# Optimization experiments

Hardware: AMD Instinct MI355X
Metric: run time of the kernel (lower is better)

Reference implementation:

```python
import jax, jax.numpy as jnp
import numpy as np
import math

IN_F, OUT_F = 4096, 4096
ORDER, TENSOR_RANK = 4, 8
LEAF_A = math.ceil(IN_F ** (1.0 / ORDER))   # 8
LEAF_B = math.ceil(OUT_F ** (1.0 / ORDER))  # 8


def setup_inputs() -> dict:
    key = jax.random.key(0)
    k1, k2, k3, k4 = jax.random.split(key, 4)
    x = jax.random.normal(k1, (8, 2048, IN_F), dtype=jnp.float32)
    weight = jax.random.normal(k2, (OUT_F, IN_F), dtype=jnp.float32) * 0.02
    bias = jax.random.normal(k3, (OUT_F,), dtype=jnp.float32) * 0.02
    # reset_parameters: gain for leaky_relu(sqrt(5)) = sqrt(2/(1+5)); std = gain / in_features**(1/order)
    gain = math.sqrt(2.0 / (1.0 + 5.0))
    std = gain / (IN_F ** (1.0 / ORDER))
    weight_leafs = jax.random.uniform(
        k4, (ORDER, TENSOR_RANK, LEAF_A, LEAF_B), dtype=jnp.float32,
        minval=-std, maxval=std)
    return {"x": x, "weight": weight, "bias": bias, "weight_leafs": weight_leafs}


def _reproduce_weight(weight_leafs):
    # Original einsum 'lij,rmn->rimjn' sums the FIRST operand over its leading
    # (rank) axis; chained through both stages + final .sum(0), every leaf is
    # summed over tensor_rank. Exact math = nested Kronecker of the rank-summed
    # leaves, sliced to [:in_features, :out_features].
    s = weight_leafs.sum(axis=1)  # (4, a, b)
    a, b = LEAF_A, LEAF_B
    z1 = jnp.einsum('ij,mn->imjn', s[0], s[1]).reshape(a * a, b * b)
    z2 = jnp.einsum('ij,mn->imjn', s[2], s[3]).reshape(a * a, b * b)
    zzz = jnp.einsum('ij,mn->imjn', z1, z2).reshape(a ** 4, b ** 4)
    return zzz[:IN_F, :OUT_F]  # (in_features, out_features)


def reference(x, weight, bias, weight_leafs):
    tensor_weight = _reproduce_weight(weight_leafs)       # (in, out)
    full_weight = weight + tensor_weight.T                # (out, in)
    # F.linear: x @ W^T + b
    return jnp.einsum('bsi,oi->bso', x, full_weight) + bias
```

## Files before the change

kernel.cpp:

```cpp
#include <hip/hip_runtime.h>
#include <hip/hip_bf16.h>
#include <stdint.h>

typedef __attribute__((ext_vector_type(8))) __bf16 bf16x8;
typedef __attribute__((ext_vector_type(4))) float f32x4;

#define IN_F   4096
#define OUT_F  4096
#define M_ROWS 16384

static __device__ __forceinline__ unsigned short f2bf(float f) {
    unsigned int u = __float_as_uint(f);
    u += 0x7FFFu + ((u >> 16) & 1u);
    return (unsigned short)(u >> 16);
}

#define PREP_WBLK 1366
#define PREP_NBLK 4096

__global__ __launch_bounds__(256) void prep_kernel(
    const float* __restrict__ weight, const float* __restrict__ leafs,
    const float* __restrict__ x,
    unsigned short* __restrict__ wb, unsigned short* __restrict__ xbuf)
{
    const int t = threadIdx.x;
    if (blockIdx.x < PREP_WBLK) {
        __shared__ float s[4][8][8];
        {
            const int o = t >> 6, a = (t >> 3) & 7, b = t & 7;
            float acc = 0.f;
            #pragma unroll
            for (int r = 0; r < 8; ++r)
                acc += leafs[o * 512 + r * 64 + a * 8 + b];
            s[o][a][b] = acc;
        }
        __syncthreads();

        const int total = (OUT_F * IN_F) / 8;
        for (int idx = blockIdx.x * 256 + t; idx < total; idx += PREP_WBLK * 256) {
            const int n  = idx >> 9;
            const int kg = idx & 511;
            const int n0 = n >> 9, n1 = (n >> 6) & 7, n2 = (n >> 3) & 7, n3 = n & 7;
            const int k0 = kg >> 6, k1 = (kg >> 3) & 7, k2 = kg & 7;
            const float p = s[0][k0][n0] * s[1][k1][n1] * s[2][k2][n2];
            const float4* wp = (const float4*)(weight + (size_t)n * IN_F + kg * 8);
            const float4 w0 = wp[0], w1 = wp[1];
            const float wv[8] = {w0.x, w0.y, w0.z, w0.w, w1.x, w1.y, w1.z, w1.w};
            unsigned int pk[4];
            #pragma unroll
            for (int j = 0; j < 4; ++j) {
                unsigned int lo = f2bf(wv[2*j]   + p * s[3][2*j]  [n3]);
                unsigned int hi = f2bf(wv[2*j+1] + p * s[3][2*j+1][n3]);
                pk[j] = lo | (hi << 16);
            }
            *reinterpret_cast<uint4*>(wb + (size_t)n * IN_F + kg * 8) =
                make_uint4(pk[0], pk[1], pk[2], pk[3]);
        }
    } else {
        const long long n8 = (long long)M_ROWS * IN_F / 8;
        const int xblocks = PREP_NBLK - PREP_WBLK;
        for (long long idx = (long long)(blockIdx.x - PREP_WBLK) * 256 + t;
             idx < n8; idx += (long long)xblocks * 256) {
            const float4* xp = (const float4*)(x + idx * 8);
            const float4 a = xp[0], b = xp[1];
            const float v[8] = {a.x, a.y, a.z, a.w, b.x, b.y, b.z, b.w};
            unsigned int pk[4];
            #pragma unroll
            for (int j = 0; j < 4; ++j)
                pk[j] = (unsigned int)f2bf(v[2*j]) | ((unsigned int)f2bf(v[2*j+1]) << 16);
            *reinterpret_cast<uint4*>(xbuf + idx * 8) =
                make_uint4(pk[0], pk[1], pk[2], pk[3]);
        }
    }
}

#define BK 64
#define NT 64

#define PANEL_A(b,kk) (ldsb + ((b)*2+(kk))*16384)
#define PANEL_B(b,kk) (ldsb + 65536 + ((b)*2+(kk))*16384)

#define GLL(src, dst) __builtin_amdgcn_global_load_lds( \
    (const __attribute__((address_space(1))) void*)(src), \
    (__attribute__((address_space(3))) void*)(dst), 16, 0, 0)

#define STAGE_A(b, kk, ko) do { \
    GLL(sA1 + (ko) + (kk)*32,          PANEL_A(b,kk) + d1); \
    GLL(sA1 + 524288 + (ko) + (kk)*32, PANEL_A(b,kk) + d1 + 8192); } while(0)
#define STAGE_B(b, kk, ko) do { \
    GLL(sB1 + (ko) + (kk)*32,          PANEL_B(b,kk) + d1); \
    GLL(sB1 + 524288 + (ko) + (kk)*32, PANEL_B(b,kk) + d1 + 8192); } while(0)

#define SB0  __builtin_amdgcn_sched_barrier(0)
#define BAR  __builtin_amdgcn_s_barrier()
#define PRI1 __builtin_amdgcn_s_setprio(1)
#define PRI0 __builtin_amdgcn_s_setprio(0)
#define WLG4 asm volatile("s_waitcnt lgkmcnt(4)" ::: "memory")
#define WLG8 asm volatile("s_waitcnt lgkmcnt(8)" ::: "memory")
#define WLG0 asm volatile("s_waitcnt lgkmcnt(0)" ::: "memory")
#define WVM2 asm volatile("s_waitcnt vmcnt(2)" ::: "memory")
#define WVM0 asm volatile("s_waitcnt vmcnt(0)" ::: "memory")

#define LDA(dst, BUF, KK, MH) do { _Pragma("unroll") \
    for (int i_ = 0; i_ < 4; ++i_) \
        dst[i_] = *(const bf16x8*)(aB + ((BUF)*32768 + (KK)*16384 + ((MH)*4+i_)*1024)); } while(0)
#define LDB(dst, BUF, KK) do { _Pragma("unroll") \
    for (int i_ = 0; i_ < 4; ++i_) \
        dst[i_] = *(const bf16x8*)(bB + ((BUF)*32768 + (KK)*16384 + i_*1024)); } while(0)
#define MMB(AS, BS, MH) do { _Pragma("unroll") \
    for (int m_ = 0; m_ < 4; ++m_) { _Pragma("unroll") \
    for (int n_ = 0; n_ < 4; ++n_) \
        acc[(MH)*4+m_][n_] = __builtin_amdgcn_mfma_f32_16x16x32_bf16( \
            AS[m_], BS[n_], acc[(MH)*4+m_][n_], 0, 0, 0); } } while(0)

#define TILE(BUF, KO, PF) do { \
     \
    LDA(aQ, BUF, 0, 1); \
    if (PF) STAGE_A((BUF)^1, 0, KO); \
    SB0; WLG4; SB0; \
    PRI1; MMB(aP, bP, 0); PRI0; SB0; \
    if (PF) { WVM2; } else { WVM0; } \
    BAR; SB0; \
     \
    LDA(aP, BUF, 1, 0); \
    LDB(bQ, BUF, 1); \
    if (PF) STAGE_B((BUF)^1, 0, KO); \
    SB0; WLG8; SB0; \
    PRI1; MMB(aQ, bP, 1); PRI0; SB0; \
    BAR; SB0; \
     \
    LDA(aQ, BUF, 1, 1); \
    if (PF) STAGE_A((BUF)^1, 1, KO); \
    SB0; WLG4; SB0; \
    PRI1; MMB(aP, bQ, 0); PRI0; SB0; \
    if (PF) { WVM2; } else { WVM0; } \
    BAR; SB0; \
     \
    if (PF) { LDA(aP, (BUF)^1, 0, 0); LDB(bP, (BUF)^1, 0); STAGE_B((BUF)^1, 1, KO); SB0; WLG8; } \
    else    { SB0; WLG0; } \
    SB0; \
    PRI1; MMB(aQ, bQ, 1); PRI0; SB0; \
    BAR; SB0; \
} while (0)

__global__ __launch_bounds__(512, 2) void gemm8_kernel(
    const unsigned short* __restrict__ xb,
    const unsigned short* __restrict__ wb,
    const float* __restrict__ bias,
    float* __restrict__ out)
{
    __shared__ unsigned short lds_us[65536];
    char* const ldsb = (char*)lds_us;

    const int t    = threadIdx.x;
    const int wave = t >> 6;
    const int lane = t & 63;
    const int lr   = lane & 15;
    const int kq   = lane >> 4;
    const int wr   = wave >> 2;
    const int wcn  = wave & 3;
    const int sx   = (lr & 6) << 3;

    const int bid  = blockIdx.x;
    const int swzb = (bid & 7) * 128 + (bid >> 3);
    const int bm   = (swzb >> 4) * 256;
    const int bn   = (swzb & 15) * 256;

    const int c1 = t;
    const int r1 = c1 >> 2;
    const int q1 = ((c1 & 3) * 16) ^ ((r1 & 6) << 3);
    const unsigned short* sA1 = xb + (size_t)(bm + r1) * IN_F + (q1 >> 1);
    const unsigned short* sB1 = wb + (size_t)(bn + r1) * IN_F + (q1 >> 1);
    const int d1 = c1 * 16;

    const char* aB = ldsb + (wr * 128 + lr) * 64 + ((kq * 16) ^ sx);
    const char* bB = ldsb + 65536 + (wcn * 64 + lr) * 64 + ((kq * 16) ^ sx);

    f32x4 acc[8][4] = {};
    bf16x8 aP[4], aQ[4], bP[4], bQ[4];

    STAGE_A(0, 0, 0); STAGE_B(0, 0, 0); STAGE_A(0, 1, 0); STAGE_B(0, 1, 0);
    asm volatile("s_waitcnt vmcnt(4)" ::: "memory");
    BAR; SB0;
    LDA(aP, 0, 0, 0);
    LDB(bP, 0, 0);

    #pragma unroll 1
    for (int tt = 0; tt < NT - 2; tt += 2) {
        const int ko0 = (tt + 1) * BK;
        const int ko1 = (tt + 2) * BK;
        TILE(0, ko0, true);
        TILE(1, ko1, true);
    }
    TILE(0, (NT - 1) * BK, true);
    TILE(1, 0, false);

    #pragma unroll
    for (int n = 0; n < 4; ++n) {
        const int col = bn + wcn * 64 + n * 16 + lr;
        const float bv = bias[col];
        #pragma unroll
        for (int m = 0; m < 8; ++m) {
            const size_t rb = (size_t)(bm + wr * 128 + m * 16 + kq * 4) * OUT_F + col;
            #pragma unroll
            for (int j = 0; j < 4; ++j)
                out[rb + (size_t)j * OUT_F] = acc[m][n][j] + bv;
        }
    }
}

#define FBM 128
#define FBN 128
#define FBK 32

__global__ __launch_bounds__(256) void gemm_fb_kernel(
    const float* __restrict__ xf,
    const unsigned short* __restrict__ wb,
    const float* __restrict__ bias,
    float* __restrict__ out)
{
    __shared__ unsigned short As[FBM * FBK];
    __shared__ unsigned short Bs[FBN * FBK];

    const int t    = threadIdx.x;
    const int wave = t >> 6;
    const int lane = t & 63;
    const int lr   = lane & 15;
    const int kq   = lane >> 4;
    const int wr   = wave >> 1;
    const int wc   = wave & 1;

    const int bm = blockIdx.x * FBM;
    const int bn = blockIdx.y * FBN;
    const int srow = t >> 2;
    const int scol = (t & 3) * 8;

    f32x4 acc[4][4] = {};

    for (int kt = 0; kt < IN_F; kt += FBK) {
        #pragma unroll
        for (int g = 0; g < 2; ++g) {
            const int row = srow + g * 64;
            const float4* xp = (const float4*)(xf + (size_t)(bm + row) * IN_F + kt + scol);
            const float4 a0 = xp[0], a1 = xp[1];
            const float v[8] = {a0.x, a0.y, a0.z, a0.w, a1.x, a1.y, a1.z, a1.w};
            unsigned int pk[4];
            #pragma unroll
            for (int j = 0; j < 4; ++j)
                pk[j] = (unsigned int)f2bf(v[2*j]) | ((unsigned int)f2bf(v[2*j+1]) << 16);
            *reinterpret_cast<uint4*>(&As[row * FBK + scol]) =
                make_uint4(pk[0], pk[1], pk[2], pk[3]);
        }
        {
            const unsigned short* gb0 = wb + (size_t)(bn + srow) * IN_F + kt + scol;
            const unsigned short* gb1 = gb0 + (size_t)64 * IN_F;
            GLL(gb0, Bs + srow * FBK + scol);
            GLL(gb1, Bs + (64 + srow) * FBK + scol);
        }
        __syncthreads();

        bf16x8 af[4], bfr[4];
        #pragma unroll
        for (int m = 0; m < 4; ++m)
            af[m] = *reinterpret_cast<const bf16x8*>(As + (wr * 64 + m * 16 + lr) * FBK + kq * 8);
        #pragma unroll
        for (int n = 0; n < 4; ++n)
            bfr[n] = *reinterpret_cast<const bf16x8*>(Bs + (wc * 64 + n * 16 + lr) * FBK + kq * 8);

        #pragma unroll
        for (int m = 0; m < 4; ++m)
            #pragma unroll
            for (int n = 0; n < 4; ++n)
                acc[m][n] = __builtin_amdgcn_mfma_f32_16x16x32_bf16(af[m], bfr[n], acc[m][n], 0, 0, 0);

        __syncthreads();
    }

    const int crow0 = kq * 4;
    #pragma unroll
    for (int n = 0; n < 4; ++n) {
        const int col = bn + wc * 64 + n * 16 + lr;
        const float bv = bias[col];
        #pragma unroll
        for (int m = 0; m < 4; ++m) {
            const int rowb = bm + wr * 64 + m * 16 + crow0;
            #pragma unroll
            for (int j = 0; j < 4; ++j)
                out[(size_t)(rowb + j) * OUT_F + col] = acc[m][n][j] + bv;
        }
    }
}

extern "C" void kernel_launch(void* const* d_in, const int* in_sizes, int n_in,
                              void* d_out, int out_size, void* d_ws, size_t ws_size,
                              hipStream_t stream) {
    const float* x      = (const float*)d_in[0];
    const float* weight = (const float*)d_in[1];
    const float* bias   = (const float*)d_in[2];
    const float* leafs  = (const float*)d_in[3];
    float* out = (float*)d_out;

    unsigned short* wb = (unsigned short*)d_ws;
    unsigned short* xbuf = (unsigned short*)((char*)d_ws +
                           (size_t)OUT_F * IN_F * sizeof(unsigned short));

    const size_t need_full = (size_t)OUT_F * IN_F * 2 + (size_t)M_ROWS * IN_F * 2;
    const bool full = ws_size >= need_full;

    if (full) {
        prep_kernel<<<dim3(PREP_NBLK), dim3(256), 0, stream>>>(
            weight, leafs, x, wb, xbuf);
        gemm8_kernel<<<dim3((M_ROWS / 256) * (OUT_F / 256)), dim3(512), 0, stream>>>(
            xbuf, wb, bias, out);
    } else {
        prep_kernel<<<dim3(PREP_WBLK), dim3(256), 0, stream>>>(
            weight, leafs, x, wb, xbuf);
        gemm_fb_kernel<<<dim3(M_ROWS / FBM, OUT_F / FBN), dim3(256), 0, stream>>>(
            x, wb, bias, out);
    }
}
```

Measured before the change: 594.1 us.

## Switch GEMM main loop to 32x32x16 MFMA with new LDS layout and schedule

Replaces the 16x16x32 bf16 MFMA tiling with 32x32x16 MFMA fragments. This requires a new per-row XOR-swizzled LDS layout with 128-byte rows and a new staging address scheme. The per-tile pipeline is simplified to full lgkmcnt(0) waits and one vmcnt(0) per tile instead of the finer-grained partial waits used before. Larger MFMA tiles cut LDS fragment reads per FLOP, but the coarser synchronization may expose more memory latency.

```diff
diff --git a/kernel.cpp b/kernel.cpp
--- a/kernel.cpp
+++ b/kernel.cpp
@@ -2,8 +2,9 @@
 #include <hip/hip_bf16.h>
 #include <stdint.h>
 
-typedef __attribute__((ext_vector_type(8))) __bf16 bf16x8;
-typedef __attribute__((ext_vector_type(4))) float f32x4;
+typedef __attribute__((ext_vector_type(8)))  __bf16 bf16x8;
+typedef __attribute__((ext_vector_type(4)))  float  f32x4;
+typedef __attribute__((ext_vector_type(16))) float  f32x16;
 
 #define IN_F   4096
 #define OUT_F  4096
@@ -77,73 +78,63 @@
 #define BK 64
 #define NT 64
 
-#define PANEL_A(b,kk) (ldsb + ((b)*2+(kk))*16384)
-#define PANEL_B(b,kk) (ldsb + 65536 + ((b)*2+(kk))*16384)
-
 #define GLL(src, dst) __builtin_amdgcn_global_load_lds( \
     (const __attribute__((address_space(1))) void*)(src), \
     (__attribute__((address_space(3))) void*)(dst), 16, 0, 0)
-
-#define STAGE_A(b, kk, ko) do { \
-    GLL(sA1 + (ko) + (kk)*32,          PANEL_A(b,kk) + d1); \
-    GLL(sA1 + 524288 + (ko) + (kk)*32, PANEL_A(b,kk) + d1 + 8192); } while(0)
-#define STAGE_B(b, kk, ko) do { \
-    GLL(sB1 + (ko) + (kk)*32,          PANEL_B(b,kk) + d1); \
-    GLL(sB1 + 524288 + (ko) + (kk)*32, PANEL_B(b,kk) + d1 + 8192); } while(0)
 
 #define SB0  __builtin_amdgcn_sched_barrier(0)
 #define BAR  __builtin_amdgcn_s_barrier()
 #define PRI1 __builtin_amdgcn_s_setprio(1)
 #define PRI0 __builtin_amdgcn_s_setprio(0)
-#define WLG4 asm volatile("s_waitcnt lgkmcnt(4)" ::: "memory")
-#define WLG8 asm volatile("s_waitcnt lgkmcnt(8)" ::: "memory")
 #define WLG0 asm volatile("s_waitcnt lgkmcnt(0)" ::: "memory")
-#define WVM2 asm volatile("s_waitcnt vmcnt(2)" ::: "memory")
 #define WVM0 asm volatile("s_waitcnt vmcnt(0)" ::: "memory")
 
-#define LDA(dst, BUF, KK, MH) do { _Pragma("unroll") \
-    for (int i_ = 0; i_ < 4; ++i_) \
-        dst[i_] = *(const bf16x8*)(aB + ((BUF)*32768 + (KK)*16384 + ((MH)*4+i_)*1024)); } while(0)
-#define LDB(dst, BUF, KK) do { _Pragma("unroll") \
-    for (int i_ = 0; i_ < 4; ++i_) \
-        dst[i_] = *(const bf16x8*)(bB + ((BUF)*32768 + (KK)*16384 + i_*1024)); } while(0)
-#define MMB(AS, BS, MH) do { _Pragma("unroll") \
-    for (int m_ = 0; m_ < 4; ++m_) { _Pragma("unroll") \
-    for (int n_ = 0; n_ < 4; ++n_) \
-        acc[(MH)*4+m_][n_] = __builtin_amdgcn_mfma_f32_16x16x32_bf16( \
-            AS[m_], BS[n_], acc[(MH)*4+m_][n_], 0, 0, 0); } } while(0)
-
-#define TILE(BUF, KO, PF) do { \
+#define STAGE_A(b, h, ko) do { \
+    GLL(pA[h] + (ko),             ldsb + (b)*32768 + (h)*16384 + t*16); \
+    GLL(pA[h] + 64*IN_F + (ko),   ldsb + (b)*32768 + (h)*16384 + t*16 + 8192); } while(0)
+#define STAGE_B(b, h, ko) do { \
+    GLL(pB[h] + (ko),             ldsb + 65536 + (b)*32768 + (h)*16384 + t*16); \
+    GLL(pB[h] + 64*IN_F + (ko),   ldsb + 65536 + (b)*32768 + (h)*16384 + t*16 + 8192); } while(0)
+
+#define ARD(Q, KH) do { _Pragma("unroll") \
+    for (int i_ = 0; i_ < 2; ++i_) { _Pragma("unroll") \
+    for (int j_ = 0; j_ < 2; ++j_) \
+        aF[i_][j_] = *(const bf16x8*)(aPan + ((Q)*2 + i_)*4096 + \
+                     (aOff ^ ((((KH)*2 + j_)) << 5))); } } while(0)
+#define BRD(KH) do { _Pragma("unroll") \
+    for (int n_ = 0; n_ < 2; ++n_) { _Pragma("unroll") \
+    for (int j_ = 0; j_ < 2; ++j_) \
+        bFr[n_][j_] = *(const bf16x8*)(bPan + n_*4096 + \
+                      (bOff ^ ((((KH)*2 + j_)) << 5))); } } while(0)
+#define MM32(Q) do { _Pragma("unroll") \
+    for (int i_ = 0; i_ < 2; ++i_) { _Pragma("unroll") \
+    for (int n_ = 0; n_ < 2; ++n_) { _Pragma("unroll") \
+    for (int j_ = 0; j_ < 2; ++j_) \
+        acc[(Q)*2 + i_][n_] = __builtin_amdgcn_mfma_f32_32x32x16_bf16( \
+            aF[i_][j_], bFr[n_][j_], acc[(Q)*2 + i_][n_], 0, 0, 0); } } } while(0)
+
+#define TILE32(BUF, KO, PF) do { \
+    const char* aPan = ldsb + (BUF)*32768 + wr*16384; \
+    const char* bPan = ldsb + 65536 + (BUF)*32768 + (wcn >> 1)*16384; \
      \
-    LDA(aQ, BUF, 0, 1); \
-    if (PF) STAGE_A((BUF)^1, 0, KO); \
-    SB0; WLG4; SB0; \
-    PRI1; MMB(aP, bP, 0); PRI0; SB0; \
-    if (PF) { WVM2; } else { WVM0; } \
-    BAR; SB0; \
+    ARD(0, 0); BRD(0); \
+    if (PF) { STAGE_A((BUF)^1, 0, KO); STAGE_A((BUF)^1, 1, KO); } \
+    BAR; WLG0; SB0; PRI1; MM32(0); PRI0; BAR; \
      \
-    LDA(aP, BUF, 1, 0); \
-    LDB(bQ, BUF, 1); \
-    if (PF) STAGE_B((BUF)^1, 0, KO); \
-    SB0; WLG8; SB0; \
-    PRI1; MMB(aQ, bP, 1); PRI0; SB0; \
-    BAR; SB0; \
+    ARD(1, 0); \
+    if (PF) { STAGE_B((BUF)^1, 0, KO); STAGE_B((BUF)^1, 1, KO); } \
+    BAR; WLG0; SB0; PRI1; MM32(1); PRI0; BAR; \
      \
-    LDA(aQ, BUF, 1, 1); \
-    if (PF) STAGE_A((BUF)^1, 1, KO); \
-    SB0; WLG4; SB0; \
-    PRI1; MMB(aP, bQ, 0); PRI0; SB0; \
-    if (PF) { WVM2; } else { WVM0; } \
-    BAR; SB0; \
+    ARD(0, 1); BRD(1); \
+    BAR; WLG0; SB0; PRI1; MM32(0); PRI0; BAR; \
      \
-    if (PF) { LDA(aP, (BUF)^1, 0, 0); LDB(bP, (BUF)^1, 0); STAGE_B((BUF)^1, 1, KO); SB0; WLG8; } \
-    else    { SB0; WLG0; } \
-    SB0; \
-    PRI1; MMB(aQ, bQ, 1); PRI0; SB0; \
-    BAR; SB0; \
+    ARD(1, 1); \
+    BAR; WLG0; SB0; PRI1; MM32(1); PRI0; \
+    if (PF) { WVM0; } \
+    BAR; \
 } while (0)
 
-__global__ __launch_bounds__(512, 2) void gemm8_kernel(
+__global__ __launch_bounds__(512, 2) void gemm32_kernel(
     const unsigned short* __restrict__ xb,
     const unsigned short* __restrict__ wb,
     const float* __restrict__ bias,
@@ -155,56 +146,55 @@
     const int t    = threadIdx.x;
     const int wave = t >> 6;
     const int lane = t & 63;
-    const int lr   = lane & 15;
-    const int kq   = lane >> 4;
+    const int ln31 = lane & 31;
+    const int lhi  = lane >> 5;
     const int wr   = wave >> 2;
     const int wcn  = wave & 3;
-    const int sx   = (lr & 6) << 3;
 
     const int bid  = blockIdx.x;
     const int swzb = (bid & 7) * 128 + (bid >> 3);
     const int bm   = (swzb >> 4) * 256;
     const int bn   = (swzb & 15) * 256;
 
-    const int c1 = t;
-    const int r1 = c1 >> 2;
-    const int q1 = ((c1 & 3) * 16) ^ ((r1 & 6) << 3);
-    const unsigned short* sA1 = xb + (size_t)(bm + r1) * IN_F + (q1 >> 1);
-    const unsigned short* sB1 = wb + (size_t)(bn + r1) * IN_F + (q1 >> 1);
-    const int d1 = c1 * 16;
-
-    const char* aB = ldsb + (wr * 128 + lr) * 64 + ((kq * 16) ^ sx);
-    const char* bB = ldsb + 65536 + (wcn * 64 + lr) * 64 + ((kq * 16) ^ sx);
-
-    f32x4 acc[8][4] = {};
-    bf16x8 aP[4], aQ[4], bP[4], bQ[4];
-
-    STAGE_A(0, 0, 0); STAGE_B(0, 0, 0); STAGE_A(0, 1, 0); STAGE_B(0, 1, 0);
-    asm volatile("s_waitcnt vmcnt(4)" ::: "memory");
-    BAR; SB0;
-    LDA(aP, 0, 0, 0);
-    LDB(bP, 0, 0);
+    const int r1  = t >> 3;
+    const int slp = (t & 7) ^ (r1 & 7);
+    const unsigned short* pA[2] = {
+        xb + (size_t)(bm + r1) * IN_F + slp * 8,
+        xb + (size_t)(bm + 128 + r1) * IN_F + slp * 8 };
+    const unsigned short* pB[2] = {
+        wb + (size_t)(bn + r1) * IN_F + slp * 8,
+        wb + (size_t)(bn + 128 + r1) * IN_F + slp * 8 };
+
+    const int c0   = ((lhi ^ (ln31 & 7)) << 4);
+    const int aOff = ln31 * 128 + c0;
+    const int bOff = ((wcn & 1) * 64 + ln31) * 128 + c0;
+
+    f32x16 acc[4][2] = {};
+    bf16x8 aF[2][2], bFr[2][2];
+
+    STAGE_A(0, 0, 0); STAGE_A(0, 1, 0); STAGE_B(0, 0, 0); STAGE_B(0, 1, 0);
+    WVM0; BAR;
 
     #pragma unroll 1
     for (int tt = 0; tt < NT - 2; tt += 2) {
-        const int ko0 = (tt + 1) * BK;
-        const int ko1 = (tt + 2) * BK;
-        TILE(0, ko0, true);
-        TILE(1, ko1, true);
-    }
-    TILE(0, (NT - 1) * BK, true);
-    TILE(1, 0, false);
+        TILE32(0, (tt + 1) * BK, true);
+        TILE32(1, (tt + 2) * BK, true);
+    }
+    TILE32(0, (NT - 1) * BK, true);
+    TILE32(1, 0, false);
 
     #pragma unroll
-    for (int n = 0; n < 4; ++n) {
-        const int col = bn + wcn * 64 + n * 16 + lr;
+    for (int fn = 0; fn < 2; ++fn) {
+        const int col = bn + wcn * 64 + fn * 32 + ln31;
         const float bv = bias[col];
         #pragma unroll
-        for (int m = 0; m < 8; ++m) {
-            const size_t rb = (size_t)(bm + wr * 128 + m * 16 + kq * 4) * OUT_F + col;
-            #pragma unroll
-            for (int j = 0; j < 4; ++j)
-                out[rb + (size_t)j * OUT_F] = acc[m][n][j] + bv;
+        for (int fm = 0; fm < 4; ++fm) {
+            const int rb = bm + wr * 128 + fm * 32 + 4 * lhi;
+            #pragma unroll
+            for (int reg = 0; reg < 16; ++reg) {
+                const int row = rb + (reg & 3) + 8 * (reg >> 2);
+                out[(size_t)row * OUT_F + col] = acc[fm][fn][reg] + bv;
+            }
         }
     }
 }
@@ -310,7 +300,7 @@
     if (full) {
         prep_kernel<<<dim3(PREP_NBLK), dim3(256), 0, stream>>>(
             weight, leafs, x, wb, xbuf);
-        gemm8_kernel<<<dim3((M_ROWS / 256) * (OUT_F / 256)), dim3(512), 0, stream>>>(
+        gemm32_kernel<<<dim3((M_ROWS / 256) * (OUT_F / 256)), dim3(512), 0, stream>>>(
             xbuf, wb, bias, out);
     } else {
         prep_kernel<<<dim3(PREP_WBLK), dim3(256), 0, stream>>>(
```

After: 616.1 us. 1.04x slower.

## Restructure GEMM main loop into two half-tile phases with one barrier each

Applied to the files above, without the earlier changes.

Replaces the four-phase-per-tile software pipeline (ping-pong A/B register fragments, four barriers per K tile) with a simpler two-half schedule. Each half issues its prefetch of the next stage, loads A and B fragments from LDS, and runs two 4x4 MFMA groups split by an lgkmcnt wait. This halves the number of barriers per tile and drops the cross-phase register prefetch. In exchange it exposes more LDS-load latency before the MFMAs and weakens the overlap of global prefetch with compute.

```diff
diff --git a/kernel.cpp b/kernel.cpp
--- a/kernel.cpp
+++ b/kernel.cpp
@@ -96,54 +96,41 @@
 #define PRI1 __builtin_amdgcn_s_setprio(1)
 #define PRI0 __builtin_amdgcn_s_setprio(0)
 #define WLG4 asm volatile("s_waitcnt lgkmcnt(4)" ::: "memory")
-#define WLG8 asm volatile("s_waitcnt lgkmcnt(8)" ::: "memory")
 #define WLG0 asm volatile("s_waitcnt lgkmcnt(0)" ::: "memory")
-#define WVM2 asm volatile("s_waitcnt vmcnt(2)" ::: "memory")
+#define WVM4 asm volatile("s_waitcnt vmcnt(4)" ::: "memory")
 #define WVM0 asm volatile("s_waitcnt vmcnt(0)" ::: "memory")
 
-#define LDA(dst, BUF, KK, MH) do { _Pragma("unroll") \
+#define HALF(P, KK, KO, PF) do { \
+    if (PF) { STAGE_A((P)^1, KK, KO); STAGE_B((P)^1, KK, KO); } \
+    _Pragma("unroll") \
     for (int i_ = 0; i_ < 4; ++i_) \
-        dst[i_] = *(const bf16x8*)(aB + ((BUF)*32768 + (KK)*16384 + ((MH)*4+i_)*1024)); } while(0)
-#define LDB(dst, BUF, KK) do { _Pragma("unroll") \
+        aG1[i_] = *(const bf16x8*)(aB + (P)*32768 + (KK)*16384 + i_*1024); \
+    _Pragma("unroll") \
     for (int i_ = 0; i_ < 4; ++i_) \
-        dst[i_] = *(const bf16x8*)(bB + ((BUF)*32768 + (KK)*16384 + i_*1024)); } while(0)
-#define MMB(AS, BS, MH) do { _Pragma("unroll") \
+        bG[i_]  = *(const bf16x8*)(bB + (P)*32768 + (KK)*16384 + i_*1024); \
+    _Pragma("unroll") \
+    for (int i_ = 0; i_ < 4; ++i_) \
+        aG2[i_] = *(const bf16x8*)(aB + (P)*32768 + (KK)*16384 + (4+i_)*1024); \
+    SB0; WLG4; SB0; \
+    PRI1; \
+    _Pragma("unroll") \
     for (int m_ = 0; m_ < 4; ++m_) { _Pragma("unroll") \
     for (int n_ = 0; n_ < 4; ++n_) \
-        acc[(MH)*4+m_][n_] = __builtin_amdgcn_mfma_f32_16x16x32_bf16( \
-            AS[m_], BS[n_], acc[(MH)*4+m_][n_], 0, 0, 0); } } while(0)
-
-#define TILE(BUF, KO, PF) do { \
-     \
-    LDA(aQ, BUF, 0, 1); \
-    if (PF) STAGE_A((BUF)^1, 0, KO); \
-    SB0; WLG4; SB0; \
-    PRI1; MMB(aP, bP, 0); PRI0; SB0; \
-    if (PF) { WVM2; } else { WVM0; } \
-    BAR; SB0; \
-     \
-    LDA(aP, BUF, 1, 0); \
-    LDB(bQ, BUF, 1); \
-    if (PF) STAGE_B((BUF)^1, 0, KO); \
-    SB0; WLG8; SB0; \
-    PRI1; MMB(aQ, bP, 1); PRI0; SB0; \
-    BAR; SB0; \
-     \
-    LDA(aQ, BUF, 1, 1); \
-    if (PF) STAGE_A((BUF)^1, 1, KO); \
-    SB0; WLG4; SB0; \
-    PRI1; MMB(aP, bQ, 0); PRI0; SB0; \
-    if (PF) { WVM2; } else { WVM0; } \
-    BAR; SB0; \
-     \
-    if (PF) { LDA(aP, (BUF)^1, 0, 0); LDB(bP, (BUF)^1, 0); STAGE_B((BUF)^1, 1, KO); SB0; WLG8; } \
-    else    { SB0; WLG0; } \
-    SB0; \
-    PRI1; MMB(aQ, bQ, 1); PRI0; SB0; \
+        acc[m_][n_] = __builtin_amdgcn_mfma_f32_16x16x32_bf16( \
+            aG1[m_], bG[n_], acc[m_][n_], 0, 0, 0); } \
+    PRI0; SB0; WLG0; SB0; \
+    PRI1; \
+    _Pragma("unroll") \
+    for (int m_ = 0; m_ < 4; ++m_) { _Pragma("unroll") \
+    for (int n_ = 0; n_ < 4; ++n_) \
+        acc[4+m_][n_] = __builtin_amdgcn_mfma_f32_16x16x32_bf16( \
+            aG2[m_], bG[n_], acc[4+m_][n_], 0, 0, 0); } \
+    PRI0; SB0; \
+    if (PF) { WVM4; } else { WVM0; } \
     BAR; SB0; \
 } while (0)
 
-__global__ __launch_bounds__(512, 2) void gemm8_kernel(
+__global__ __launch_bounds__(512, 2) void gemm2b_kernel(
     const unsigned short* __restrict__ xb,
     const unsigned short* __restrict__ wb,
     const float* __restrict__ bias,
@@ -177,23 +164,20 @@
     const char* bB = ldsb + 65536 + (wcn * 64 + lr) * 64 + ((kq * 16) ^ sx);
 
     f32x4 acc[8][4] = {};
-    bf16x8 aP[4], aQ[4], bP[4], bQ[4];
+    bf16x8 aG1[4], aG2[4], bG[4];
 
     STAGE_A(0, 0, 0); STAGE_B(0, 0, 0); STAGE_A(0, 1, 0); STAGE_B(0, 1, 0);
-    asm volatile("s_waitcnt vmcnt(4)" ::: "memory");
-    BAR; SB0;
-    LDA(aP, 0, 0, 0);
-    LDB(bP, 0, 0);
+    WVM4; BAR; SB0;
 
     #pragma unroll 1
-    for (int tt = 0; tt < NT - 2; tt += 2) {
-        const int ko0 = (tt + 1) * BK;
-        const int ko1 = (tt + 2) * BK;
-        TILE(0, ko0, true);
-        TILE(1, ko1, true);
-    }
-    TILE(0, (NT - 1) * BK, true);
-    TILE(1, 0, false);
+    for (int tt = 0; tt < NT - 1; ++tt) {
+        const int p  = tt & 1;
+        const int ko = (tt + 1) * BK;
+        HALF(p, 0, ko, true);
+        HALF(p, 1, ko, true);
+    }
+    HALF(1, 0, 0, false);
+    HALF(1, 1, 0, false);
 
     #pragma unroll
     for (int n = 0; n < 4; ++n) {
@@ -310,7 +294,7 @@
     if (full) {
         prep_kernel<<<dim3(PREP_NBLK), dim3(256), 0, stream>>>(
             weight, leafs, x, wb, xbuf);
-        gemm8_kernel<<<dim3((M_ROWS / 256) * (OUT_F / 256)), dim3(512), 0, stream>>>(
+        gemm2b_kernel<<<dim3((M_ROWS / 256) * (OUT_F / 256)), dim3(512), 0, stream>>>(
             xbuf, wb, bias, out);
     } else {
         prep_kernel<<<dim3(PREP_WBLK), dim3(256), 0, stream>>>(
```

Measured after the change: 587.7 us. Within noise of the previous version (-1.1%).
